# Optimization experiments

Measured on AMD Instinct MI355X. Metric: run time of the kernel, lower is better.

Reference implementation:

```python
import jax, jax.numpy as jnp
import numpy as np

EPS = 1e-8

def setup_inputs() -> dict:
    key = jax.random.key(0)
    ks = jax.random.split(key, 4)
    B, N, D, H = 8, 4096, 768, 256
    x = jax.random.normal(ks[0], (B, N, D), dtype=jnp.float32)
    W_base = jnp.ones((N, D), dtype=jnp.float32)
    modrelu_bias = jnp.full((D,), -0.1, dtype=jnp.float32)
    mlp_w1 = jax.random.normal(ks[1], (D, H), dtype=jnp.float32) * (1.0 / np.sqrt(D))
    mlp_b1 = jnp.zeros((H,), dtype=jnp.float32)
    mlp_w2 = jax.random.normal(ks[2], (H, D), dtype=jnp.float32) * (1.0 / np.sqrt(H))
    mlp_b2 = jnp.zeros((D,), dtype=jnp.float32)
    return {"x": x, "W_base": W_base, "modrelu_bias": modrelu_bias,
            "mlp_w1": mlp_w1, "mlp_b1": mlp_b1, "mlp_w2": mlp_w2, "mlp_b2": mlp_b2}

def reference(x, W_base, modrelu_bias, mlp_w1, mlp_b1, mlp_w2, mlp_b2):
    # FFT along last axis (embed_dim), matching tf.signal.fft semantics
    F = jnp.fft.fft(x.astype(jnp.complex64), axis=-1)  # (B, N, D) complex64
    # global context and adaptive filter delta
    c = jnp.mean(x, axis=1)                              # (B, D)
    h = jax.nn.gelu(c @ mlp_w1 + mlp_b1)                 # (B, H)
    delta_W = h @ mlp_w2 + mlp_b2                        # (B, D)
    W = W_base[None, :, :] + delta_W[:, None, :]         # (B, N, D)
    F_filtered = F * W.astype(jnp.complex64)
    # modReLU
    mag = jnp.abs(F_filtered)
    mag_act = jax.nn.relu(mag + modrelu_bias)
    scale = mag_act / jnp.maximum(mag, EPS)
    F_activated = F_filtered * scale.astype(jnp.complex64)
    Y = jnp.real(jnp.fft.ifft(F_activated, axis=-1)).astype(jnp.float32)
    return Y
```

## Files before the change

### kernel.cpp

```cpp
#include <hip/hip_runtime.h>
#include <math.h>

#define BDIM 8
#define NSEQ 4096
#define DDIM 768
#define HDIM 256
#define ROWS 2
#define CH 64

#define SW(a) ((a) + ((a) >> 5))
#define LDSN (DDIM + DDIM / 32)

__global__ __launch_bounds__(192)
void colsum_kernel(const float* __restrict__ x, float* __restrict__ csum) {
    int blk = blockIdx.x;
    int ch = blk % CH;
    int b  = blk / CH;
    int t  = threadIdx.x;
    const int nper = NSEQ / CH;
    const float4* p = reinterpret_cast<const float4*>(
        x + ((size_t)b * NSEQ + (size_t)ch * nper) * DDIM) + t;
    float4 acc = make_float4(0.f, 0.f, 0.f, 0.f);
    #pragma unroll 8
    for (int i = 0; i < nper; ++i) {
        float4 v = p[(size_t)i * (DDIM / 4)];
        acc.x += v.x; acc.y += v.y; acc.z += v.z; acc.w += v.w;
    }
    float* c = csum + b * DDIM + t * 4;
    atomicAdd(c + 0, acc.x);
    atomicAdd(c + 1, acc.y);
    atomicAdd(c + 2, acc.z);
    atomicAdd(c + 3, acc.w);
}

__global__ __launch_bounds__(64)
void mlp_h_kernel(const float* __restrict__ csum, const float* __restrict__ w1,
                  const float* __restrict__ b1, float* __restrict__ h) {
    const int blk = blockIdx.x;
    const int hh = blk & (HDIM - 1);
    const int b  = blk >> 8;
    const int l  = threadIdx.x;
    const float* c = csum + b * DDIM;
    const float* w = w1 + hh;
    float acc = 0.f;
    #pragma unroll
    for (int j = 0; j < 12; ++j) {
        int d = l * 12 + j;
        acc = fmaf(c[d], w[(size_t)d * HDIM], acc);
    }
    #pragma unroll
    for (int off = 32; off; off >>= 1) acc += __shfl_down(acc, off);
    if (l == 0) {
        float a = acc * (1.0f / NSEQ) + b1[hh];
        float x3 = a * a * a;
        float g = 0.5f * a * (1.0f + tanhf(0.7978845608028654f * (a + 0.044715f * x3)));
        h[b * HDIM + hh] = g;
    }
}

__global__ __launch_bounds__(64)
void mlp_dw_kernel(const float* __restrict__ h, const float* __restrict__ w2,
                   float* __restrict__ dW) {
    const int blk = blockIdx.x;
    const int dc = blk % 12;
    const int jc = (blk / 12) & 3;
    const int b  = blk / 48;
    const int l  = threadIdx.x;
    __shared__ float hs[64];
    hs[l] = h[b * HDIM + jc * 64 + l];
    __syncthreads();
    const int d = dc * 64 + l;
    const float* w = w2 + (size_t)(jc * 64) * DDIM + d;
    float acc = 0.f;
    #pragma unroll 8
    for (int j = 0; j < 64; ++j) acc = fmaf(hs[j], w[(size_t)j * DDIM], acc);
    atomicAdd(&dW[b * DDIM + d], acc);
}

template <int R, int S, int M, bool INV>
__device__ __forceinline__ void fft_stage(
    const float* __restrict__ sre, const float* __restrict__ sim,
    float* __restrict__ dre, float* __restrict__ dim_,
    const float* __restrict__ twr, const float* __restrict__ twi, int lane)
{
    constexpr int NB = S * M;
    #pragma unroll
    for (int it = 0; it < NB / 64; ++it) {
        const int id = lane + 64 * it;
        const int u  = id / S;
        const int sg = id - u * S;
        const int ob = u * R * S + sg;
        if constexpr (R == 4) {
            float x0r = sre[SW(id)],          x0i = sim[SW(id)];
            float x1r = sre[SW(NB + id)],     x1i = sim[SW(NB + id)];
            float x2r = sre[SW(2 * NB + id)], x2i = sim[SW(2 * NB + id)];
            float x3r = sre[SW(3 * NB + id)], x3i = sim[SW(3 * NB + id)];
            float t0r = x0r + x2r, t0i = x0i + x2i;
            float t1r = x0r - x2r, t1i = x0i - x2i;
            float t2r = x1r + x3r, t2i = x1i + x3i;
            float t3r = x1r - x3r, t3i = x1i - x3i;
            float A0r = t0r + t2r, A0i = t0i + t2i;
            float A2r = t0r - t2r, A2i = t0i - t2i;
            float A1r, A1i, A3r, A3i;
            if constexpr (!INV) {
                A1r = t1r + t3i; A1i = t1i - t3r;
                A3r = t1r - t3i; A3i = t1i + t3r;
            } else {
                A1r = t1r - t3i; A1i = t1i + t3r;
                A3r = t1r + t3i; A3i = t1i - t3r;
            }
            if constexpr (M > 1) {
                const int e = u * S;
                float w1r = twr[e],     w1i = twi[e];
                float w2r = twr[2 * e], w2i = twi[2 * e];
                float w3r = twr[3 * e], w3i = twi[3 * e];
                if constexpr (INV) { w1i = -w1i; w2i = -w2i; w3i = -w3i; }
                float r1 = A1r * w1r - A1i * w1i, i1 = A1r * w1i + A1i * w1r;
                float r2 = A2r * w2r - A2i * w2i, i2 = A2r * w2i + A2i * w2r;
                float r3 = A3r * w3r - A3i * w3i, i3 = A3r * w3i + A3i * w3r;
                A1r = r1; A1i = i1; A2r = r2; A2i = i2; A3r = r3; A3i = i3;
            }
            dre[SW(ob)]         = A0r; dim_[SW(ob)]         = A0i;
            dre[SW(ob + S)]     = A1r; dim_[SW(ob + S)]     = A1i;
            dre[SW(ob + 2 * S)] = A2r; dim_[SW(ob + 2 * S)] = A2i;
            dre[SW(ob + 3 * S)] = A3r; dim_[SW(ob + 3 * S)] = A3i;
        } else {
            float x0r = sre[SW(id)],          x0i = sim[SW(id)];
            float x1r = sre[SW(NB + id)],     x1i = sim[SW(NB + id)];
            float x2r = sre[SW(2 * NB + id)], x2i = sim[SW(2 * NB + id)];
            float tr = x1r + x2r, ti = x1i + x2i;
            float ur = x1r - x2r, ui = x1i - x2i;
            constexpr float C3 = -0.5f;
            constexpr float S3 = INV ? 0.8660254037844386f : -0.8660254037844386f;
            float br = x0r + C3 * tr, bi = x0i + C3 * ti;
            float A0r = x0r + tr, A0i = x0i + ti;
            float A1r = br - S3 * ui, A1i = bi + S3 * ur;
            float A2r = br + S3 * ui, A2i = bi - S3 * ur;
            if constexpr (M > 1) {
                const int e = u * S;
                float w1r = twr[e],     w1i = twi[e];
                float w2r = twr[2 * e], w2i = twi[2 * e];
                if constexpr (INV) { w1i = -w1i; w2i = -w2i; }
                float r1 = A1r * w1r - A1i * w1i, i1 = A1r * w1i + A1i * w1r;
                float r2 = A2r * w2r - A2i * w2i, i2 = A2r * w2i + A2i * w2r;
                A1r = r1; A1i = i1; A2r = r2; A2i = i2;
            }
            dre[SW(ob)]         = A0r; dim_[SW(ob)]         = A0i;
            dre[SW(ob + S)]     = A1r; dim_[SW(ob + S)]     = A1i;
            dre[SW(ob + 2 * S)] = A2r; dim_[SW(ob + 2 * S)] = A2i;
        }
    }
}

__device__ __forceinline__ float geff(float w, float m, float b) {
    float mag = fabsf(w) * m;
    float mact = fmaxf(mag + b, 0.0f);
    return w * (mact / fmaxf(mag, 1e-8f));
}

__global__ __launch_bounds__(64 * ROWS)
void fftmix_kernel(const float* __restrict__ x, const float* __restrict__ Wb,
                   const float* __restrict__ dW, const float* __restrict__ bias,
                   const float* __restrict__ b2, float* __restrict__ out) {
    __shared__ float twr[DDIM], twi[DDIM];
    __shared__ float Are[ROWS][LDSN], Aim[ROWS][LDSN];
    __shared__ float Bre[ROWS][LDSN], Bim[ROWS][LDSN];

    const int t = threadIdx.x;
    for (int j = t; j < DDIM; j += 64 * ROWS) {
        float s, c;
        __sincosf(-(6.283185307179586f / DDIM) * (float)j, &s, &c);
        twr[j] = c; twi[j] = s;
    }

    const int w = t >> 6, lane = t & 63;
    const int pair = blockIdx.x * ROWS + w;
    const int r1 = 2 * pair;
    const int b  = r1 >> 12;
    const int n1 = r1 & (NSEQ - 1);

    float* are = Are[w]; float* aim = Aim[w];
    float* bre = Bre[w]; float* bim = Bim[w];

    const float* x1 = x + (size_t)r1 * DDIM;
    const float* x2 = x1 + DDIM;
    #pragma unroll
    for (int q = 0; q < 3; ++q) {
        int c4 = lane + 64 * q;
        float4 v1 = reinterpret_cast<const float4*>(x1)[c4];
        float4 v2 = reinterpret_cast<const float4*>(x2)[c4];
        int j = 4 * c4;
        are[SW(j + 0)] = v1.x; are[SW(j + 1)] = v1.y;
        are[SW(j + 2)] = v1.z; are[SW(j + 3)] = v1.w;
        aim[SW(j + 0)] = v2.x; aim[SW(j + 1)] = v2.y;
        aim[SW(j + 2)] = v2.z; aim[SW(j + 3)] = v2.w;
    }
    __syncthreads();

    fft_stage<4, 1, 192, false>(are, aim, bre, bim, twr, twi, lane); __syncthreads();
    fft_stage<4, 4, 48, false>(bre, bim, are, aim, twr, twi, lane); __syncthreads();
    fft_stage<4, 16, 12, false>(are, aim, bre, bim, twr, twi, lane); __syncthreads();
    fft_stage<4, 64, 3, false>(bre, bim, are, aim, twr, twi, lane); __syncthreads();
    fft_stage<3, 256, 1, false>(are, aim, bre, bim, twr, twi, lane); __syncthreads();

    {
        const float* wb1 = Wb + (size_t)n1 * DDIM;
        const float* wb2 = wb1 + DDIM;
        const float* dwr = dW + (size_t)b * DDIM;
        auto process = [&](int k) {
            int nk = (k == 0) ? 0 : DDIM - k;
            float Zkr = bre[SW(k)],  Zki = bim[SW(k)];
            float Znr = bre[SW(nk)], Zni = bim[SW(nk)];
            float F1r = 0.5f * (Zkr + Znr), F1i = 0.5f * (Zki - Zni);
            float F2r = 0.5f * (Zki + Zni), F2i = 0.5f * (Znr - Zkr);
            float m1 = sqrtf(F1r * F1r + F1i * F1i);
            float m2 = sqrtf(F2r * F2r + F2i * F2i);
            float dk = dwr[k] + b2[k],  dn = dwr[nk] + b2[nk];
            float bk = bias[k], bn = bias[nk];
            float w1k = wb1[k] + dk, w1n = wb1[nk] + dn;
            float w2k = wb2[k] + dk, w2n = wb2[nk] + dn;
            float g1 = 0.5f * (geff(w1k, m1, bk) + geff(w1n, m1, bn));
            float g2 = 0.5f * (geff(w2k, m2, bk) + geff(w2n, m2, bn));
            bre[SW(k)]  = g1 * F1r - g2 * F2i;
            bim[SW(k)]  = g1 * F1i + g2 * F2r;
            bre[SW(nk)] = g1 * F1r + g2 * F2i;
            bim[SW(nk)] = -g1 * F1i + g2 * F2r;
        };
        #pragma unroll
        for (int q = 0; q < 6; ++q) process(lane + 64 * q);
        if (lane == 0) process(384);
    }
    __syncthreads();

    fft_stage<4, 1, 192, true>(bre, bim, are, aim, twr, twi, lane); __syncthreads();
    fft_stage<4, 4, 48, true>(are, aim, bre, bim, twr, twi, lane); __syncthreads();
    fft_stage<4, 16, 12, true>(bre, bim, are, aim, twr, twi, lane); __syncthreads();
    fft_stage<4, 64, 3, true>(are, aim, bre, bim, twr, twi, lane); __syncthreads();
    fft_stage<3, 256, 1, true>(bre, bim, are, aim, twr, twi, lane); __syncthreads();

    float* o1 = out + (size_t)r1 * DDIM;
    float* o2 = o1 + DDIM;
    constexpr float inv = 1.0f / DDIM;
    #pragma unroll
    for (int q = 0; q < 3; ++q) {
        int c4 = lane + 64 * q;
        int j = 4 * c4;
        float4 v1 = make_float4(are[SW(j + 0)], are[SW(j + 1)],
                                are[SW(j + 2)], are[SW(j + 3)]);
        float4 v2 = make_float4(aim[SW(j + 0)], aim[SW(j + 1)],
                                aim[SW(j + 2)], aim[SW(j + 3)]);
        v1.x *= inv; v1.y *= inv; v1.z *= inv; v1.w *= inv;
        v2.x *= inv; v2.y *= inv; v2.z *= inv; v2.w *= inv;
        reinterpret_cast<float4*>(o1)[c4] = v1;
        reinterpret_cast<float4*>(o2)[c4] = v2;
    }
}

extern "C" void kernel_launch(void* const* d_in, const int* in_sizes, int n_in,
                              void* d_out, int out_size, void* d_ws, size_t ws_size,
                              hipStream_t stream) {
    const float* x    = (const float*)d_in[0];
    const float* Wb   = (const float*)d_in[1];
    const float* bias = (const float*)d_in[2];
    const float* w1   = (const float*)d_in[3];
    const float* b1   = (const float*)d_in[4];
    const float* w2   = (const float*)d_in[5];
    const float* b2   = (const float*)d_in[6];
    float* out = (float*)d_out;

    float* csum = (float*)d_ws;
    float* dW   = csum + BDIM * DDIM;
    float* h    = dW + BDIM * DDIM;

    hipMemsetAsync(d_ws, 0, 2 * BDIM * DDIM * sizeof(float), stream);
    colsum_kernel<<<BDIM * CH, 192, 0, stream>>>(x, csum);
    mlp_h_kernel<<<BDIM * HDIM, 64, 0, stream>>>(csum, w1, b1, h);
    mlp_dw_kernel<<<BDIM * 4 * 12, 64, 0, stream>>>(h, w2, dW);
    fftmix_kernel<<<(BDIM * NSEQ / 2) / ROWS, 64 * ROWS, 0, stream>>>(x, Wb, dW, bias, b2, out);
}
```

Baseline: 137.9 us.

## Replace LDS-staged FFT with register-resident wave-shuffle FFT using DPP/swizzle

Result: slower. 145.3 us (+5.3%).

```diff
diff --git a/kernel.cpp b/kernel.cpp
--- a/kernel.cpp
+++ b/kernel.cpp
@@ -5,11 +5,7 @@
 #define NSEQ 4096
 #define DDIM 768
 #define HDIM 256
-#define ROWS 2
 #define CH 64
-
-#define SW(a) ((a) + ((a) >> 5))
-#define LDSN (DDIM + DDIM / 32)
 
 __global__ __launch_bounds__(192)
 void colsum_kernel(const float* __restrict__ x, float* __restrict__ csum) {
@@ -31,6 +27,12 @@
     atomicAdd(c + 1, acc.y);
     atomicAdd(c + 2, acc.z);
     atomicAdd(c + 3, acc.w);
+}
+
+__global__ __launch_bounds__(256)
+void dwinit_kernel(const float* __restrict__ b2, float* __restrict__ dW) {
+    int idx = blockIdx.x * 256 + threadIdx.x;
+    dW[idx] = b2[idx % DDIM];
 }
 
 __global__ __launch_bounds__(64)
@@ -77,78 +79,109 @@
     atomicAdd(&dW[b * DDIM + d], acc);
 }
 
-template <int R, int S, int M, bool INV>
-__device__ __forceinline__ void fft_stage(
-    const float* __restrict__ sre, const float* __restrict__ sim,
-    float* __restrict__ dre, float* __restrict__ dim_,
-    const float* __restrict__ twr, const float* __restrict__ twi, int lane)
-{
-    constexpr int NB = S * M;
-    #pragma unroll
-    for (int it = 0; it < NB / 64; ++it) {
-        const int id = lane + 64 * it;
-        const int u  = id / S;
-        const int sg = id - u * S;
-        const int ob = u * R * S + sg;
-        if constexpr (R == 4) {
-            float x0r = sre[SW(id)],          x0i = sim[SW(id)];
-            float x1r = sre[SW(NB + id)],     x1i = sim[SW(NB + id)];
-            float x2r = sre[SW(2 * NB + id)], x2i = sim[SW(2 * NB + id)];
-            float x3r = sre[SW(3 * NB + id)], x3i = sim[SW(3 * NB + id)];
-            float t0r = x0r + x2r, t0i = x0i + x2i;
-            float t1r = x0r - x2r, t1i = x0i - x2i;
-            float t2r = x1r + x3r, t2i = x1i + x3i;
-            float t3r = x1r - x3r, t3i = x1i - x3i;
-            float A0r = t0r + t2r, A0i = t0i + t2i;
-            float A2r = t0r - t2r, A2i = t0i - t2i;
-            float A1r, A1i, A3r, A3i;
-            if constexpr (!INV) {
-                A1r = t1r + t3i; A1i = t1i - t3r;
-                A3r = t1r - t3i; A3i = t1i + t3r;
-            } else {
-                A1r = t1r - t3i; A1i = t1i + t3r;
-                A3r = t1r + t3i; A3i = t1i - t3r;
-            }
-            if constexpr (M > 1) {
-                const int e = u * S;
-                float w1r = twr[e],     w1i = twi[e];
-                float w2r = twr[2 * e], w2i = twi[2 * e];
-                float w3r = twr[3 * e], w3i = twi[3 * e];
-                if constexpr (INV) { w1i = -w1i; w2i = -w2i; w3i = -w3i; }
-                float r1 = A1r * w1r - A1i * w1i, i1 = A1r * w1i + A1i * w1r;
-                float r2 = A2r * w2r - A2i * w2i, i2 = A2r * w2i + A2i * w2r;
-                float r3 = A3r * w3r - A3i * w3i, i3 = A3r * w3i + A3i * w3r;
-                A1r = r1; A1i = i1; A2r = r2; A2i = i2; A3r = r3; A3i = i3;
-            }
-            dre[SW(ob)]         = A0r; dim_[SW(ob)]         = A0i;
-            dre[SW(ob + S)]     = A1r; dim_[SW(ob + S)]     = A1i;
-            dre[SW(ob + 2 * S)] = A2r; dim_[SW(ob + 2 * S)] = A2i;
-            dre[SW(ob + 3 * S)] = A3r; dim_[SW(ob + 3 * S)] = A3i;
+
+__device__ __forceinline__ void cmulc(float& r, float& i, float br, float bi) {
+    float tr = r * br - i * bi;
+    float ti = r * bi + i * br;
+    r = tr; i = ti;
+}
+
+template<int M>
+__device__ __forceinline__ float xsh(float v, int l) {
+    int iv = __float_as_int(v);
+    if constexpr (M == 1)       iv = __builtin_amdgcn_mov_dpp(iv, 0xB1, 0xF, 0xF, false);
+    else if constexpr (M == 2)  iv = __builtin_amdgcn_mov_dpp(iv, 0x4E, 0xF, 0xF, false);
+    else if constexpr (M == 32) iv = __builtin_amdgcn_ds_bpermute((l ^ 32) << 2, iv);
+    else                        iv = __builtin_amdgcn_ds_swizzle(iv, (M << 10) | 0x1F);
+    return __int_as_float(iv);
+}
+
+template<int M>
+__device__ __forceinline__ void stage_fwd(float* zr, float* zi, int l) {
+    float wc = 1.f, ws = 0.f;
+    if constexpr (M > 1) {
+        float jj = (float)(l & (M - 1));
+        __sincosf(-(3.14159265358979323846f / M) * jj, &ws, &wc);
+    }
+    const bool hi = (l & M) != 0;
+    const float sgn = hi ? -1.f : 1.f;
+    #pragma unroll
+    for (int j = 0; j < 12; ++j) {
+        float pr = xsh<M>(zr[j], l), pi = xsh<M>(zi[j], l);
+        float er = hi ? zr[j] : pr,  ei = hi ? zi[j] : pi;
+        float o_r = hi ? pr : zr[j], o_i = hi ? pi : zi[j];
+        float tr, ti;
+        if constexpr (M > 1) { tr = wc * er - ws * ei; ti = wc * ei + ws * er; }
+        else                 { tr = er; ti = ei; }
+        zr[j] = fmaf(sgn, tr, o_r);
+        zi[j] = fmaf(sgn, ti, o_i);
+    }
+}
+
+template<int M>
+__device__ __forceinline__ void stage_inv(float* zr, float* zi, int l) {
+    float wc = 1.f, ws = 0.f;
+    if constexpr (M > 1) {
+        float jj = (float)(l & (M - 1));
+        __sincosf((3.14159265358979323846f / M) * jj, &ws, &wc);
+    }
+    const bool hi = (l & M) != 0;
+    const float sgn = hi ? -1.f : 1.f;
+    const float wc2 = hi ? wc : 1.f;
+    const float ws2 = hi ? ws : 0.f;
+    #pragma unroll
+    for (int j = 0; j < 12; ++j) {
+        float pr = xsh<M>(zr[j], l), pi = xsh<M>(zi[j], l);
+        float tr = fmaf(sgn, zr[j], pr);
+        float ti = fmaf(sgn, zi[j], pi);
+        zr[j] = wc2 * tr - ws2 * ti;
+        zi[j] = wc2 * ti + ws2 * tr;
+    }
+}
+
+template<bool INV>
+__device__ __forceinline__ void dft12(float* zr, float* zi) {
+    constexpr float C1 = 0.8660254037844386f;
+    constexpr float SG = INV ? 1.f : -1.f;
+    constexpr float E  = INV ? -C1 : C1;
+    float sr[3][4], si[3][4];
+    #pragma unroll
+    for (int b = 0; b < 3; ++b) {
+        float x0r = zr[b],     x0i = zi[b];
+        float x1r = zr[3 + b], x1i = zi[3 + b];
+        float x2r = zr[6 + b], x2i = zi[6 + b];
+        float x3r = zr[9 + b], x3i = zi[9 + b];
+        float t0r = x0r + x2r, t0i = x0i + x2i;
+        float t1r = x0r - x2r, t1i = x0i - x2i;
+        float t2r = x1r + x3r, t2i = x1i + x3i;
+        float t3r = x1r - x3r, t3i = x1i - x3i;
+        sr[b][0] = t0r + t2r; si[b][0] = t0i + t2i;
+        sr[b][2] = t0r - t2r; si[b][2] = t0i - t2i;
+        if constexpr (!INV) {
+            sr[b][1] = t1r + t3i; si[b][1] = t1i - t3r;
+            sr[b][3] = t1r - t3i; si[b][3] = t1i + t3r;
         } else {
-            float x0r = sre[SW(id)],          x0i = sim[SW(id)];
-            float x1r = sre[SW(NB + id)],     x1i = sim[SW(NB + id)];
-            float x2r = sre[SW(2 * NB + id)], x2i = sim[SW(2 * NB + id)];
-            float tr = x1r + x2r, ti = x1i + x2i;
-            float ur = x1r - x2r, ui = x1i - x2i;
-            constexpr float C3 = -0.5f;
-            constexpr float S3 = INV ? 0.8660254037844386f : -0.8660254037844386f;
-            float br = x0r + C3 * tr, bi = x0i + C3 * ti;
-            float A0r = x0r + tr, A0i = x0i + ti;
-            float A1r = br - S3 * ui, A1i = bi + S3 * ur;
-            float A2r = br + S3 * ui, A2i = bi - S3 * ur;
-            if constexpr (M > 1) {
-                const int e = u * S;
-                float w1r = twr[e],     w1i = twi[e];
-                float w2r = twr[2 * e], w2i = twi[2 * e];
-                if constexpr (INV) { w1i = -w1i; w2i = -w2i; }
-                float r1 = A1r * w1r - A1i * w1i, i1 = A1r * w1i + A1i * w1r;
-                float r2 = A2r * w2r - A2i * w2i, i2 = A2r * w2i + A2i * w2r;
-                A1r = r1; A1i = i1; A2r = r2; A2i = i2;
-            }
-            dre[SW(ob)]         = A0r; dim_[SW(ob)]         = A0i;
-            dre[SW(ob + S)]     = A1r; dim_[SW(ob + S)]     = A1i;
-            dre[SW(ob + 2 * S)] = A2r; dim_[SW(ob + 2 * S)] = A2i;
-        }
+            sr[b][1] = t1r - t3i; si[b][1] = t1i + t3r;
+            sr[b][3] = t1r + t3i; si[b][3] = t1i - t3r;
+        }
+    }
+    cmulc(sr[1][1], si[1][1], C1,  SG * 0.5f);
+    cmulc(sr[1][2], si[1][2], 0.5f, SG * C1);
+    { float t = sr[1][3]; sr[1][3] = -SG * si[1][3]; si[1][3] = SG * t; }
+    cmulc(sr[2][1], si[2][1], 0.5f,  SG * C1);
+    cmulc(sr[2][2], si[2][2], -0.5f, SG * C1);
+    sr[2][3] = -sr[2][3]; si[2][3] = -si[2][3];
+    #pragma unroll
+    for (int p = 0; p < 4; ++p) {
+        float x0r = sr[0][p], x0i = si[0][p];
+        float x1r = sr[1][p], x1i = si[1][p];
+        float x2r = sr[2][p], x2i = si[2][p];
+        float tr = x1r + x2r, ti = x1i + x2i;
+        float ur = x1r - x2r, ui = x1i - x2i;
+        float br = x0r - 0.5f * tr, bi = x0i - 0.5f * ti;
+        zr[p]     = x0r + tr;        zi[p]     = x0i + ti;
+        zr[4 + p] = br + E * ui;     zi[4 + p] = bi - E * ur;
+        zr[8 + p] = br - E * ui;     zi[8 + p] = bi + E * ur;
     }
 }
 
@@ -158,101 +191,109 @@
     return w * (mact / fmaxf(mag, 1e-8f));
 }
 
-__global__ __launch_bounds__(64 * ROWS)
+__global__ __launch_bounds__(256)
 void fftmix_kernel(const float* __restrict__ x, const float* __restrict__ Wb,
                    const float* __restrict__ dW, const float* __restrict__ bias,
-                   const float* __restrict__ b2, float* __restrict__ out) {
-    __shared__ float twr[DDIM], twi[DDIM];
-    __shared__ float Are[ROWS][LDSN], Aim[ROWS][LDSN];
-    __shared__ float Bre[ROWS][LDSN], Bim[ROWS][LDSN];
-
-    const int t = threadIdx.x;
-    for (int j = t; j < DDIM; j += 64 * ROWS) {
-        float s, c;
-        __sincosf(-(6.283185307179586f / DDIM) * (float)j, &s, &c);
-        twr[j] = c; twi[j] = s;
-    }
-
-    const int w = t >> 6, lane = t & 63;
-    const int pair = blockIdx.x * ROWS + w;
-    const int r1 = 2 * pair;
-    const int b  = r1 >> 12;
-    const int n1 = r1 & (NSEQ - 1);
-
-    float* are = Are[w]; float* aim = Aim[w];
-    float* bre = Bre[w]; float* bim = Bim[w];
-
-    const float* x1 = x + (size_t)r1 * DDIM;
-    const float* x2 = x1 + DDIM;
-    #pragma unroll
-    for (int q = 0; q < 3; ++q) {
-        int c4 = lane + 64 * q;
-        float4 v1 = reinterpret_cast<const float4*>(x1)[c4];
-        float4 v2 = reinterpret_cast<const float4*>(x2)[c4];
-        int j = 4 * c4;
-        are[SW(j + 0)] = v1.x; are[SW(j + 1)] = v1.y;
-        are[SW(j + 2)] = v1.z; are[SW(j + 3)] = v1.w;
-        aim[SW(j + 0)] = v2.x; aim[SW(j + 1)] = v2.y;
-        aim[SW(j + 2)] = v2.z; aim[SW(j + 3)] = v2.w;
-    }
-    __syncthreads();
-
-    fft_stage<4, 1, 192, false>(are, aim, bre, bim, twr, twi, lane); __syncthreads();
-    fft_stage<4, 4, 48, false>(bre, bim, are, aim, twr, twi, lane); __syncthreads();
-    fft_stage<4, 16, 12, false>(are, aim, bre, bim, twr, twi, lane); __syncthreads();
-    fft_stage<4, 64, 3, false>(bre, bim, are, aim, twr, twi, lane); __syncthreads();
-    fft_stage<3, 256, 1, false>(are, aim, bre, bim, twr, twi, lane); __syncthreads();
-
-    {
-        const float* wb1 = Wb + (size_t)n1 * DDIM;
+                   float* __restrict__ out) {
+    const int l  = threadIdx.x & 63;
+    const int wv = threadIdx.x >> 6;
+    const int pair = blockIdx.x * 4 + wv;
+    const int r1 = pair * 2;
+    const int bb = r1 >> 12;
+    const int sq = r1 & (NSEQ - 1);
+    const int rl = __brev((unsigned)l) >> 26;
+
+    float zr[12], zi[12];
+    {
+        const float4* p1 = reinterpret_cast<const float4*>(x + (size_t)r1 * DDIM + 12 * rl);
+        const float4* p2 = reinterpret_cast<const float4*>(x + (size_t)(r1 + 1) * DDIM + 12 * rl);
+        float4 a0 = p1[0], a1 = p1[1], a2 = p1[2];
+        float4 b0 = p2[0], b1_ = p2[1], b2_ = p2[2];
+        zr[0] = a0.x; zr[1] = a0.y; zr[2] = a0.z; zr[3] = a0.w;
+        zr[4] = a1.x; zr[5] = a1.y; zr[6] = a1.z; zr[7] = a1.w;
+        zr[8] = a2.x; zr[9] = a2.y; zr[10] = a2.z; zr[11] = a2.w;
+        zi[0] = b0.x; zi[1] = b0.y; zi[2] = b0.z; zi[3] = b0.w;
+        zi[4] = b1_.x; zi[5] = b1_.y; zi[6] = b1_.z; zi[7] = b1_.w;
+        zi[8] = b2_.x; zi[9] = b2_.y; zi[10] = b2_.z; zi[11] = b2_.w;
+    }
+
+    stage_fwd<1>(zr, zi, l);  stage_fwd<2>(zr, zi, l);  stage_fwd<4>(zr, zi, l);
+    stage_fwd<8>(zr, zi, l);  stage_fwd<16>(zr, zi, l); stage_fwd<32>(zr, zi, l);
+
+    {
+        float cb, sb;
+        __sincosf(-(6.283185307179586f / DDIM) * (float)l, &sb, &cb);
+        float wr = cb, wi = sb;
+        cmulc(zr[1], zi[1], wr, wi);
+        #pragma unroll
+        for (int j = 2; j < 12; ++j) {
+            cmulc(wr, wi, cb, sb);
+            cmulc(zr[j], zi[j], wr, wi);
+        }
+    }
+
+    dft12<false>(zr, zi);
+
+    {
+        float shr[12], shi[12];
+        const int src = ((64 - l) & 63) << 2;
+        #pragma unroll
+        for (int j = 0; j < 12; ++j) {
+            shr[j] = __int_as_float(__builtin_amdgcn_ds_bpermute(src, __float_as_int(zr[j])));
+            shi[j] = __int_as_float(__builtin_amdgcn_ds_bpermute(src, __float_as_int(zi[j])));
+        }
+        const float* wb1 = Wb + (size_t)sq * DDIM;
         const float* wb2 = wb1 + DDIM;
-        const float* dwr = dW + (size_t)b * DDIM;
-        auto process = [&](int k) {
-            int nk = (k == 0) ? 0 : DDIM - k;
-            float Zkr = bre[SW(k)],  Zki = bim[SW(k)];
-            float Znr = bre[SW(nk)], Zni = bim[SW(nk)];
+        const float* dwb = dW + (size_t)bb * DDIM;
+        #pragma unroll
+        for (int k1 = 0; k1 < 12; ++k1) {
+            const int kx = 64 * k1 + l;
+            const int nk = kx ? (DDIM - kx) : 0;
+            float Znr = (l == 0) ? shr[(12 - k1) % 12] : shr[11 - k1];
+            float Zni = (l == 0) ? shi[(12 - k1) % 12] : shi[11 - k1];
+            float Zkr = zr[k1], Zki = zi[k1];
             float F1r = 0.5f * (Zkr + Znr), F1i = 0.5f * (Zki - Zni);
             float F2r = 0.5f * (Zki + Zni), F2i = 0.5f * (Znr - Zkr);
             float m1 = sqrtf(F1r * F1r + F1i * F1i);
             float m2 = sqrtf(F2r * F2r + F2i * F2i);
-            float dk = dwr[k] + b2[k],  dn = dwr[nk] + b2[nk];
-            float bk = bias[k], bn = bias[nk];
-            float w1k = wb1[k] + dk, w1n = wb1[nk] + dn;
-            float w2k = wb2[k] + dk, w2n = wb2[nk] + dn;
+            float dk = dwb[kx], dn = dwb[nk];
+            float bk = bias[kx], bn = bias[nk];
+            float w1k = wb1[kx] + dk, w1n = wb1[nk] + dn;
+            float w2k = wb2[kx] + dk, w2n = wb2[nk] + dn;
             float g1 = 0.5f * (geff(w1k, m1, bk) + geff(w1n, m1, bn));
             float g2 = 0.5f * (geff(w2k, m2, bk) + geff(w2n, m2, bn));
-            bre[SW(k)]  = g1 * F1r - g2 * F2i;
-            bim[SW(k)]  = g1 * F1i + g2 * F2r;
-            bre[SW(nk)] = g1 * F1r + g2 * F2i;
-            bim[SW(nk)] = -g1 * F1i + g2 * F2r;
-        };
+            zr[k1] = g1 * F1r - g2 * F2i;
+            zi[k1] = g1 * F1i + g2 * F2r;
+        }
+    }
+
+    dft12<true>(zr, zi);
+
+    {
+        float cb, sb;
+        __sincosf((6.283185307179586f / DDIM) * (float)l, &sb, &cb);
+        float wr = cb, wi = sb;
+        cmulc(zr[1], zi[1], wr, wi);
         #pragma unroll
-        for (int q = 0; q < 6; ++q) process(lane + 64 * q);
-        if (lane == 0) process(384);
-    }
-    __syncthreads();
-
-    fft_stage<4, 1, 192, true>(bre, bim, are, aim, twr, twi, lane); __syncthreads();
-    fft_stage<4, 4, 48, true>(are, aim, bre, bim, twr, twi, lane); __syncthreads();
-    fft_stage<4, 16, 12, true>(bre, bim, are, aim, twr, twi, lane); __syncthreads();
-    fft_stage<4, 64, 3, true>(are, aim, bre, bim, twr, twi, lane); __syncthreads();
-    fft_stage<3, 256, 1, true>(bre, bim, are, aim, twr, twi, lane); __syncthreads();
-
-    float* o1 = out + (size_t)r1 * DDIM;
-    float* o2 = o1 + DDIM;
-    constexpr float inv = 1.0f / DDIM;
-    #pragma unroll
-    for (int q = 0; q < 3; ++q) {
-        int c4 = lane + 64 * q;
-        int j = 4 * c4;
-        float4 v1 = make_float4(are[SW(j + 0)], are[SW(j + 1)],
-                                are[SW(j + 2)], are[SW(j + 3)]);
-        float4 v2 = make_float4(aim[SW(j + 0)], aim[SW(j + 1)],
-                                aim[SW(j + 2)], aim[SW(j + 3)]);
-        v1.x *= inv; v1.y *= inv; v1.z *= inv; v1.w *= inv;
-        v2.x *= inv; v2.y *= inv; v2.z *= inv; v2.w *= inv;
-        reinterpret_cast<float4*>(o1)[c4] = v1;
-        reinterpret_cast<float4*>(o2)[c4] = v2;
+        for (int j = 2; j < 12; ++j) {
+            cmulc(wr, wi, cb, sb);
+            cmulc(zr[j], zi[j], wr, wi);
+        }
+    }
+
+    stage_inv<32>(zr, zi, l); stage_inv<16>(zr, zi, l); stage_inv<8>(zr, zi, l);
+    stage_inv<4>(zr, zi, l);  stage_inv<2>(zr, zi, l);  stage_inv<1>(zr, zi, l);
+
+    {
+        constexpr float inv = 1.0f / DDIM;
+        float4* o1 = reinterpret_cast<float4*>(out + (size_t)r1 * DDIM + 12 * rl);
+        float4* o2 = reinterpret_cast<float4*>(out + (size_t)(r1 + 1) * DDIM + 12 * rl);
+        o1[0] = make_float4(zr[0] * inv, zr[1] * inv, zr[2] * inv, zr[3] * inv);
+        o1[1] = make_float4(zr[4] * inv, zr[5] * inv, zr[6] * inv, zr[7] * inv);
+        o1[2] = make_float4(zr[8] * inv, zr[9] * inv, zr[10] * inv, zr[11] * inv);
+        o2[0] = make_float4(zi[0] * inv, zi[1] * inv, zi[2] * inv, zi[3] * inv);
+        o2[1] = make_float4(zi[4] * inv, zi[5] * inv, zi[6] * inv, zi[7] * inv);
+        o2[2] = make_float4(zi[8] * inv, zi[9] * inv, zi[10] * inv, zi[11] * inv);
     }
 }
 
@@ -272,9 +313,10 @@
     float* dW   = csum + BDIM * DDIM;
     float* h    = dW + BDIM * DDIM;
 
-    hipMemsetAsync(d_ws, 0, 2 * BDIM * DDIM * sizeof(float), stream);
+    hipMemsetAsync(csum, 0, BDIM * DDIM * sizeof(float), stream);
+    dwinit_kernel<<<(BDIM * DDIM) / 256, 256, 0, stream>>>(b2, dW);
     colsum_kernel<<<BDIM * CH, 192, 0, stream>>>(x, csum);
     mlp_h_kernel<<<BDIM * HDIM, 64, 0, stream>>>(csum, w1, b1, h);
     mlp_dw_kernel<<<BDIM * 4 * 12, 64, 0, stream>>>(h, w2, dW);
-    fftmix_kernel<<<(BDIM * NSEQ / 2) / ROWS, 64 * ROWS, 0, stream>>>(x, Wb, dW, bias, b2, out);
-}
+    fftmix_kernel<<<(BDIM * NSEQ / 2) / 4, 256, 0, stream>>>(x, Wb, dW, bias, out);
+}
```
